# Optimization experiments

Measured on AMD Instinct MI355X. Metric: run time of the kernel, lower is better.

## Reference

```python
import jax, jax.numpy as jnp
import numpy as np

MARGIN = 0.2
EPS = 1e-6  # torch.pairwise_distance default eps added to (x1 - x2)


def setup_inputs() -> dict:
    key = jax.random.key(0)
    k1, k2 = jax.random.split(key)
    N, D = 8192, 128
    x = jax.random.normal(k1, (N, D), dtype=jnp.float32)
    target = jax.random.randint(k2, (N,), 0, 1000)
    return {"x": x, "target": target}


def _pairwise_dist(x):
    # torch.pairwise_distance(x.unsqueeze(0), x.unsqueeze(1)):
    #   diff[i, j] = x[j] - x[i] + EPS ; dist[i, j] = ||diff[i, j]||_2
    # Expanded quadratic form avoids the [N, N, D] diff tensor:
    #   ||a - b + e||^2 = ||a||^2 + ||b||^2 - 2 a.b + 2e*sum(a - b) + D*e^2
    sq = jnp.sum(x * x, axis=1)          # [N]
    s = jnp.sum(x, axis=1)               # [N]
    dot = x @ x.T                        # [N, N]
    D = x.shape[1]
    d2 = (sq[None, :] + sq[:, None] - 2.0 * dot
          + 2.0 * EPS * (s[None, :] - s[:, None]) + D * EPS * EPS)
    return jnp.sqrt(jnp.maximum(d2, 0.0))


def reference(x, target):
    N = x.shape[0]
    dist = _pairwise_dist(x)                                 # [N, N]
    same = target[None, :] == target[:, None]                # [N, N] bool
    pos_mask = (same & ~jnp.eye(N, dtype=bool)).astype(x.dtype)
    hardest_pos = jnp.max(pos_mask * dist, axis=1, keepdims=True)  # [N, 1]
    neg_mask = (~same).astype(x.dtype)
    max_neg = jnp.max(dist, axis=1, keepdims=True)           # [N, 1]
    anchor_neg = dist + max_neg * (1.0 - neg_mask)           # push positives up
    hardest_neg = jnp.min(anchor_neg, axis=1, keepdims=True) # [N, 1]
    loss = jax.nn.relu(hardest_pos - hardest_neg + MARGIN)
    return jnp.mean(loss)
```

## Files before the change

### kernel.cpp

```cpp
#include <hip/hip_runtime.h>

#define N 8192
#define Dk 128
#define EPSC 1e-6f
#define MARGIN 0.2f

typedef __attribute__((ext_vector_type(8))) short bf16x8;
typedef __attribute__((ext_vector_type(4))) float f32x4;

__device__ __forceinline__ unsigned short f2bf(float f) {
    unsigned u = __float_as_uint(f);
    u = (u + 0x7FFFu + ((u >> 16) & 1u)) >> 16;
    return (unsigned short)u;
}
__device__ __forceinline__ unsigned enc(float f) {
    unsigned u = __float_as_uint(f);
    return (u & 0x80000000u) ? ~u : (u | 0x80000000u);
}
__device__ __forceinline__ float dec(unsigned u) {
    return __uint_as_float((u & 0x80000000u) ? (u & 0x7FFFFFFFu) : ~u);
}

__device__ __forceinline__ void gl_lds16(const void* src, void* lds_dst) {
    __builtin_amdgcn_global_load_lds(
        (const __attribute__((address_space(1))) unsigned*)src,
        (__attribute__((address_space(3))) unsigned*)lds_dst, 16, 0, 0);
}

__global__ void prep_kernel(const float* __restrict__ x, const int* __restrict__ tgt,
                            unsigned short* __restrict__ Xb, uint2* __restrict__ QT,
                            float* __restrict__ P,
                            unsigned* __restrict__ wsHp, unsigned* __restrict__ wsMn) {
    int row = blockIdx.x * 4 + (threadIdx.x >> 6);
    int l = threadIdx.x & 63;
    const float2 v = *reinterpret_cast<const float2*>(&x[row * Dk + l * 2]);
    float sq = fmaf(v.x, v.x, v.y * v.y);
    float s = v.x + v.y;
    ushort2 a;
    a.x = f2bf(v.x);
    a.y = f2bf(v.y);
    int c_phys = (l >> 2) ^ (row & 7);
    *reinterpret_cast<ushort2*>(&Xb[row * Dk + c_phys * 8 + 2 * (l & 3)]) = a;
#pragma unroll
    for (int m = 32; m >= 1; m >>= 1) {
        sq += __shfl_xor(sq, m);
        s += __shfl_xor(s, m);
    }
    if (l == 0) {
        P[row] = sq - 2.0f * EPSC * s;
        float Qj = sq + 2.0f * EPSC * s + (float)Dk * EPSC * EPSC;
        uint2 qt;
        qt.x = __float_as_uint(-0.5f * Qj);
        qt.y = (unsigned)tgt[row];
        QT[row] = qt;
        wsHp[row] = 0xFF800000u;
        wsMn[row] = 0x007FFFFFu;
    }
}

__global__ __launch_bounds__(256, 4) void main_kernel(
        const unsigned short* __restrict__ Xb,
        const uint2* __restrict__ QT, const int* __restrict__ tgt,
        unsigned* __restrict__ wsHp, unsigned* __restrict__ wsMn) {
    __shared__ unsigned short Bs[2][64 * Dk];
    __shared__ uint2 QTs[2][128];

    const int tid = threadIdx.x;
    const int w = tid >> 6;
    const int lane = tid & 63;
    const int n = lane & 15;
    const int q = lane >> 4;
    const int sw = n & 7;

    const int ig = (int)blockIdx.x >> 4;
    const int js = (int)blockIdx.x & 15;
    const int rbase = ig * 128 + 32 * w;

    const bf16x8* Xv = reinterpret_cast<const bf16x8*>(Xb);

    bf16x8 Af[2][4];
#pragma unroll
    for (int ti = 0; ti < 2; ++ti)
#pragma unroll
        for (int kk = 0; kk < 4; ++kk)
            Af[ti][kk] = Xv[(rbase + 16 * ti + n) * 16 + ((q + 4 * kk) ^ sw)];

    int tsl[8];
#pragma unroll
    for (int ti = 0; ti < 2; ++ti) {
        int4 t4 = *reinterpret_cast<const int4*>(&tgt[rbase + 16 * ti + 4 * q]);
        tsl[4 * ti + 0] = t4.x;
        tsl[4 * ti + 1] = t4.y;
        tsl[4 * ti + 2] = t4.z;
        tsl[4 * ti + 3] = t4.w;
    }

    float hp[8], mn[8];
#pragma unroll
    for (int s = 0; s < 8; ++s) {
        hp[s] = INFINITY;
        mn[s] = -INFINITY;
    }

    auto stage = [&](int step) {
        const int jb = js * 512 + step * 64;
        const int buf = step & 1;
#pragma unroll
        for (int t = 0; t < 4; ++t)
            gl_lds16(&Xb[(jb + 16 * w + 4 * t) * Dk] + lane * 8,
                     &Bs[buf][(16 * w + 4 * t) * Dk]);
        if (w == 0)
            gl_lds16(reinterpret_cast<const unsigned short*>(&QT[jb]) + lane * 8,
                     &QTs[buf][0]);
    };

    stage(0);

    for (int step = 0; step < 8; ++step) {
        const int buf = step & 1;
        __syncthreads();
        if (step < 7) stage(step + 1);

        float Qv[4];
        int tv[4];
#pragma unroll
        for (int tj = 0; tj < 4; ++tj) {
            uint2 qt = QTs[buf][16 * tj + n];
            Qv[tj] = __uint_as_float(qt.x);
            tv[tj] = (int)qt.y;
        }

        f32x4 acc[2][4];
#pragma unroll
        for (int ti = 0; ti < 2; ++ti)
#pragma unroll
            for (int tj = 0; tj < 4; ++tj) acc[ti][tj] = Qv[tj];

#pragma unroll
        for (int kk = 0; kk < 4; ++kk) {
            bf16x8 Bf[4];
#pragma unroll
            for (int tj = 0; tj < 4; ++tj)
                Bf[tj] = *reinterpret_cast<const bf16x8*>(
                    &Bs[buf][(16 * tj + n) * Dk + (((q + 4 * kk) ^ sw) << 3)]);
#pragma unroll
            for (int ti = 0; ti < 2; ++ti)
#pragma unroll
                for (int tj = 0; tj < 4; ++tj)
                    acc[ti][tj] = __builtin_amdgcn_mfma_f32_16x16x32_bf16(Af[ti][kk], Bf[tj],
                                                                          acc[ti][tj], 0, 0, 0);
        }

#pragma unroll
        for (int tj = 0; tj < 4; ++tj) {
            int tvv = tv[tj];
#pragma unroll
            for (int ti = 0; ti < 2; ++ti) {
                f32x4 v = acc[ti][tj];
                int e0 = tvv == tsl[4 * ti + 0];
                int e1 = tvv == tsl[4 * ti + 1];
                int e2 = tvv == tsl[4 * ti + 2];
                int e3 = tvv == tsl[4 * ti + 3];
                if (__ballot(e0 | e1 | e2 | e3)) {
                    hp[4 * ti + 0] = fminf(hp[4 * ti + 0], e0 ? v[0] : INFINITY);
                    hp[4 * ti + 1] = fminf(hp[4 * ti + 1], e1 ? v[1] : INFINITY);
                    hp[4 * ti + 2] = fminf(hp[4 * ti + 2], e2 ? v[2] : INFINITY);
                    hp[4 * ti + 3] = fminf(hp[4 * ti + 3], e3 ? v[3] : INFINITY);
                    mn[4 * ti + 0] = fmaxf(mn[4 * ti + 0], e0 ? -INFINITY : v[0]);
                    mn[4 * ti + 1] = fmaxf(mn[4 * ti + 1], e1 ? -INFINITY : v[1]);
                    mn[4 * ti + 2] = fmaxf(mn[4 * ti + 2], e2 ? -INFINITY : v[2]);
                    mn[4 * ti + 3] = fmaxf(mn[4 * ti + 3], e3 ? -INFINITY : v[3]);
                } else {
                    mn[4 * ti + 0] = fmaxf(mn[4 * ti + 0], v[0]);
                    mn[4 * ti + 1] = fmaxf(mn[4 * ti + 1], v[1]);
                    mn[4 * ti + 2] = fmaxf(mn[4 * ti + 2], v[2]);
                    mn[4 * ti + 3] = fmaxf(mn[4 * ti + 3], v[3]);
                }
            }
        }
    }

#pragma unroll
    for (int m = 1; m <= 8; m <<= 1) {
#pragma unroll
        for (int s = 0; s < 8; ++s) {
            hp[s] = fminf(hp[s], __shfl_xor(hp[s], m));
            mn[s] = fmaxf(mn[s], __shfl_xor(mn[s], m));
        }
    }
    if (n == 0) {
#pragma unroll
        for (int ti = 0; ti < 2; ++ti) {
#pragma unroll
            for (int r = 0; r < 4; ++r) {
                int i = rbase + 16 * ti + 4 * q + r;
                atomicMin(&wsHp[i], enc(hp[4 * ti + r]));
                atomicMax(&wsMn[i], enc(mn[4 * ti + r]));
            }
        }
    }
}

__global__ void finish_kernel(const float* __restrict__ P,
                              const unsigned* __restrict__ wsHp,
                              const unsigned* __restrict__ wsMn,
                              float* __restrict__ out) {
    int t = threadIdx.x;
    float sum = 0.0f;
#pragma unroll
    for (int h = 0; h < 2; ++h) {
        int base = 8 * t + 4 * h;
        float4 Pv = *reinterpret_cast<const float4*>(&P[base]);
        uint4 Hv = *reinterpret_cast<const uint4*>(&wsHp[base]);
        uint4 Mv = *reinterpret_cast<const uint4*>(&wsMn[base]);
        const float* Pf = &Pv.x;
        const unsigned* Hu = &Hv.x;
        const unsigned* Mu = &Mv.x;
#pragma unroll
        for (int k = 0; k < 4; ++k) {
            float hp = sqrtf(fmaxf(fmaf(-2.0f, dec(Hu[k]), Pf[k]), 0.0f));
            float hn = sqrtf(fmaxf(fmaf(-2.0f, dec(Mu[k]), Pf[k]), 0.0f));
            sum += fmaxf(hp - hn + MARGIN, 0.0f);
        }
    }
#pragma unroll
    for (int m = 32; m >= 1; m >>= 1) sum += __shfl_xor(sum, m);
    __shared__ float ws[16];
    if ((t & 63) == 0) ws[t >> 6] = sum;
    __syncthreads();
    if (t == 0) {
        float tot = 0.0f;
#pragma unroll
        for (int i = 0; i < 16; ++i) tot += ws[i];
        out[0] = tot * (1.0f / (float)N);
    }
}

extern "C" void kernel_launch(void* const* d_in, const int* in_sizes, int n_in,
                              void* d_out, int out_size, void* d_ws, size_t ws_size,
                              hipStream_t stream) {
    const float* x = (const float*)d_in[0];
    const int* tgt = (const int*)d_in[1];
    float* out = (float*)d_out;

    char* ws = (char*)d_ws;
    const size_t xb = (size_t)N * Dk * 2;
    unsigned short* Xb = (unsigned short*)ws;
    uint2* QT = (uint2*)(ws + xb);
    float* P = (float*)(ws + xb + (size_t)N * 8);
    unsigned* wsHp = (unsigned*)(ws + xb + (size_t)N * 12);
    unsigned* wsMn = (unsigned*)(ws + xb + (size_t)N * 16);

    prep_kernel<<<N / 4, 256, 0, stream>>>(x, tgt, Xb, QT, P, wsHp, wsMn);
    main_kernel<<<1024, 256, 0, stream>>>(Xb, QT, tgt, wsHp, wsMn);
    finish_kernel<<<1, 1024, 0, stream>>>(P, wsHp, wsMn, out);
}
```

Baseline: 96.97 us.

## Replace LDS-staged B tiles with direct global register loads in single-wave blocks

Removes the shared-memory double buffer and __syncthreads, so each single-wave block loads B fragments straight from global (L2) memory into registers, with a two-deep register prefetch across k-steps. Each wave now covers 64 anchor rows instead of 32, which doubles A-fragment reuse per B load. The grid becomes 2048 blocks of 64 threads, and the XOR swizzle in the bf16 layout is dropped since LDS is no longer used. The aim is to cut LDS traffic and barrier overhead. In exchange, register pressure rises, global/L2 load traffic per MFMA is higher with no LDS sharing between waves, and occupancy may drop.

```diff
diff --git a/kernel.cpp b/kernel.cpp
--- a/kernel.cpp
+++ b/kernel.cpp
@@ -19,12 +19,6 @@
 }
 __device__ __forceinline__ float dec(unsigned u) {
     return __uint_as_float((u & 0x80000000u) ? (u & 0x7FFFFFFFu) : ~u);
-}
-
-__device__ __forceinline__ void gl_lds16(const void* src, void* lds_dst) {
-    __builtin_amdgcn_global_load_lds(
-        (const __attribute__((address_space(1))) unsigned*)src,
-        (__attribute__((address_space(3))) unsigned*)lds_dst, 16, 0, 0);
 }
 
 __global__ void prep_kernel(const float* __restrict__ x, const int* __restrict__ tgt,
@@ -39,8 +33,7 @@
     ushort2 a;
     a.x = f2bf(v.x);
     a.y = f2bf(v.y);
-    int c_phys = (l >> 2) ^ (row & 7);
-    *reinterpret_cast<ushort2*>(&Xb[row * Dk + c_phys * 8 + 2 * (l & 3)]) = a;
+    *reinterpret_cast<ushort2*>(&Xb[row * Dk + l * 2]) = a;
 #pragma unroll
     for (int m = 32; m >= 1; m >>= 1) {
         sq += __shfl_xor(sq, m);
@@ -58,36 +51,31 @@
     }
 }
 
-__global__ __launch_bounds__(256, 4) void main_kernel(
+__global__ __launch_bounds__(64, 2) void main_kernel(
         const unsigned short* __restrict__ Xb,
         const uint2* __restrict__ QT, const int* __restrict__ tgt,
         unsigned* __restrict__ wsHp, unsigned* __restrict__ wsMn) {
-    __shared__ unsigned short Bs[2][64 * Dk];
-    __shared__ uint2 QTs[2][128];
-
-    const int tid = threadIdx.x;
-    const int w = tid >> 6;
-    const int lane = tid & 63;
+    const int lane = threadIdx.x;
     const int n = lane & 15;
     const int q = lane >> 4;
-    const int sw = n & 7;
-
-    const int ig = (int)blockIdx.x >> 4;
+
+    const int rg = (int)blockIdx.x >> 4;
     const int js = (int)blockIdx.x & 15;
-    const int rbase = ig * 128 + 32 * w;
+    const int rbase = rg * 64;
+    const int jb0 = js * 512;
 
     const bf16x8* Xv = reinterpret_cast<const bf16x8*>(Xb);
 
-    bf16x8 Af[2][4];
-#pragma unroll
-    for (int ti = 0; ti < 2; ++ti)
+    bf16x8 Af[4][4];
+#pragma unroll
+    for (int ti = 0; ti < 4; ++ti)
 #pragma unroll
         for (int kk = 0; kk < 4; ++kk)
-            Af[ti][kk] = Xv[(rbase + 16 * ti + n) * 16 + ((q + 4 * kk) ^ sw)];
-
-    int tsl[8];
-#pragma unroll
-    for (int ti = 0; ti < 2; ++ti) {
+            Af[ti][kk] = Xv[(rbase + 16 * ti + n) * 16 + (q + 4 * kk)];
+
+    int tsl[16];
+#pragma unroll
+    for (int ti = 0; ti < 4; ++ti) {
         int4 t4 = *reinterpret_cast<const int4*>(&tgt[rbase + 16 * ti + 4 * q]);
         tsl[4 * ti + 0] = t4.x;
         tsl[4 * ti + 1] = t4.y;
@@ -95,67 +83,56 @@
         tsl[4 * ti + 3] = t4.w;
     }
 
-    float hp[8], mn[8];
-#pragma unroll
-    for (int s = 0; s < 8; ++s) {
+    float hp[16], mn[16];
+#pragma unroll
+    for (int s = 0; s < 16; ++s) {
         hp[s] = INFINITY;
         mn[s] = -INFINITY;
     }
 
-    auto stage = [&](int step) {
-        const int jb = js * 512 + step * 64;
-        const int buf = step & 1;
-#pragma unroll
-        for (int t = 0; t < 4; ++t)
-            gl_lds16(&Xb[(jb + 16 * w + 4 * t) * Dk] + lane * 8,
-                     &Bs[buf][(16 * w + 4 * t) * Dk]);
-        if (w == 0)
-            gl_lds16(reinterpret_cast<const unsigned short*>(&QT[jb]) + lane * 8,
-                     &QTs[buf][0]);
-    };
-
-    stage(0);
-
     for (int step = 0; step < 8; ++step) {
-        const int buf = step & 1;
-        __syncthreads();
-        if (step < 7) stage(step + 1);
+        const int jb = jb0 + step * 64;
 
         float Qv[4];
         int tv[4];
 #pragma unroll
         for (int tj = 0; tj < 4; ++tj) {
-            uint2 qt = QTs[buf][16 * tj + n];
+            uint2 qt = QT[jb + 16 * tj + n];
             Qv[tj] = __uint_as_float(qt.x);
             tv[tj] = (int)qt.y;
         }
 
-        f32x4 acc[2][4];
-#pragma unroll
-        for (int ti = 0; ti < 2; ++ti)
+        f32x4 acc[4][4];
+#pragma unroll
+        for (int ti = 0; ti < 4; ++ti)
 #pragma unroll
             for (int tj = 0; tj < 4; ++tj) acc[ti][tj] = Qv[tj];
 
+        bf16x8 Bf[2][4];
+#pragma unroll
+        for (int tj = 0; tj < 4; ++tj)
+            Bf[0][tj] = Xv[(jb + 16 * tj + n) * 16 + q];
 #pragma unroll
         for (int kk = 0; kk < 4; ++kk) {
-            bf16x8 Bf[4];
-#pragma unroll
-            for (int tj = 0; tj < 4; ++tj)
-                Bf[tj] = *reinterpret_cast<const bf16x8*>(
-                    &Bs[buf][(16 * tj + n) * Dk + (((q + 4 * kk) ^ sw) << 3)]);
-#pragma unroll
-            for (int ti = 0; ti < 2; ++ti)
+            const int cur = kk & 1;
+            if (kk < 3) {
 #pragma unroll
                 for (int tj = 0; tj < 4; ++tj)
-                    acc[ti][tj] = __builtin_amdgcn_mfma_f32_16x16x32_bf16(Af[ti][kk], Bf[tj],
-                                                                          acc[ti][tj], 0, 0, 0);
+                    Bf[cur ^ 1][tj] = Xv[(jb + 16 * tj + n) * 16 + (q + 4 * (kk + 1))];
+            }
+#pragma unroll
+            for (int ti = 0; ti < 4; ++ti)
+#pragma unroll
+                for (int tj = 0; tj < 4; ++tj)
+                    acc[ti][tj] = __builtin_amdgcn_mfma_f32_16x16x32_bf16(
+                        Af[ti][kk], Bf[cur][tj], acc[ti][tj], 0, 0, 0);
         }
 
 #pragma unroll
         for (int tj = 0; tj < 4; ++tj) {
             int tvv = tv[tj];
 #pragma unroll
-            for (int ti = 0; ti < 2; ++ti) {
+            for (int ti = 0; ti < 4; ++ti) {
                 f32x4 v = acc[ti][tj];
                 int e0 = tvv == tsl[4 * ti + 0];
                 int e1 = tvv == tsl[4 * ti + 1];
@@ -183,14 +160,14 @@
 #pragma unroll
     for (int m = 1; m <= 8; m <<= 1) {
 #pragma unroll
-        for (int s = 0; s < 8; ++s) {
+        for (int s = 0; s < 16; ++s) {
             hp[s] = fminf(hp[s], __shfl_xor(hp[s], m));
             mn[s] = fmaxf(mn[s], __shfl_xor(mn[s], m));
         }
     }
     if (n == 0) {
 #pragma unroll
-        for (int ti = 0; ti < 2; ++ti) {
+        for (int ti = 0; ti < 4; ++ti) {
 #pragma unroll
             for (int r = 0; r < 4; ++r) {
                 int i = rbase + 16 * ti + 4 * q + r;
@@ -252,6 +229,6 @@
     unsigned* wsMn = (unsigned*)(ws + xb + (size_t)N * 16);
 
     prep_kernel<<<N / 4, 256, 0, stream>>>(x, tgt, Xb, QT, P, wsHp, wsMn);
-    main_kernel<<<1024, 256, 0, stream>>>(Xb, QT, tgt, wsHp, wsMn);
+    main_kernel<<<2048, 64, 0, stream>>>(Xb, QT, tgt, wsHp, wsMn);
     finish_kernel<<<1, 1024, 0, stream>>>(P, wsHp, wsMn, out);
 }
```

After: 111.2 us. 14.6% more time.

## Exploit distance symmetry with triangular 128x128 tile grid and column-side reductions

Applied to the files above, without the earlier changes.

Switches from a full 64x512 block tiling over the N×N distance matrix to a triangular grid of 128x128 tiles (2080 blocks), computing each off-diagonal tile once and reducing it both row-wise and column-wise, so the matrix multiply work is roughly halved. The column reductions are adjusted by each row's Q term and pushed to the global hardest-positive and hardest-negative arrays with extra atomics. The whole B tile is now loaded once instead of double-buffered. MFMA sections are wrapped in setprio, and occupancy drops to 3 blocks per CU. The trade-off is more epilogue ALU work, more shuffles and atomics, and a larger LDS footprint per block.

```diff
diff --git a/kernel.cpp b/kernel.cpp
--- a/kernel.cpp
+++ b/kernel.cpp
@@ -58,12 +58,11 @@
     }
 }
 
-__global__ __launch_bounds__(256, 4) void main_kernel(
-        const unsigned short* __restrict__ Xb,
-        const uint2* __restrict__ QT, const int* __restrict__ tgt,
+__global__ __launch_bounds__(256, 3) void main_kernel(
+        const unsigned short* __restrict__ Xb, const uint2* __restrict__ QT,
         unsigned* __restrict__ wsHp, unsigned* __restrict__ wsMn) {
-    __shared__ unsigned short Bs[2][64 * Dk];
-    __shared__ uint2 QTs[2][128];
+    __shared__ unsigned short Bs[128 * Dk];
+    __shared__ uint2 QTs[128];
 
     const int tid = threadIdx.x;
     const int w = tid >> 6;
@@ -72,11 +71,25 @@
     const int q = lane >> 4;
     const int sw = n & 7;
 
-    const int ig = (int)blockIdx.x >> 4;
-    const int js = (int)blockIdx.x & 15;
+    int t = (int)blockIdx.x;
+    int jg = (int)((sqrtf(8.0f * (float)t + 1.0f) - 1.0f) * 0.5f);
+    while ((jg + 1) * (jg + 2) / 2 <= t) ++jg;
+    while (jg * (jg + 1) / 2 > t) --jg;
+    const int ig = t - jg * (jg + 1) / 2;
+    const bool diag = (ig == jg);
+
     const int rbase = ig * 128 + 32 * w;
+    const int jbase = jg * 128;
 
     const bf16x8* Xv = reinterpret_cast<const bf16x8*>(Xb);
+
+#pragma unroll
+    for (int tt = 0; tt < 8; ++tt)
+        gl_lds16(&Xb[(jbase + 32 * w + 4 * tt) * Dk] + lane * 8,
+                 &Bs[(32 * w + 4 * tt) * Dk]);
+    if (w == 0)
+        gl_lds16(reinterpret_cast<const unsigned short*>(&QT[jbase]) + lane * 8,
+                 &QTs[0]);
 
     bf16x8 Af[2][4];
 #pragma unroll
@@ -85,14 +98,20 @@
         for (int kk = 0; kk < 4; ++kk)
             Af[ti][kk] = Xv[(rbase + 16 * ti + n) * 16 + ((q + 4 * kk) ^ sw)];
 
+    float qi[8];
     int tsl[8];
 #pragma unroll
     for (int ti = 0; ti < 2; ++ti) {
-        int4 t4 = *reinterpret_cast<const int4*>(&tgt[rbase + 16 * ti + 4 * q]);
-        tsl[4 * ti + 0] = t4.x;
-        tsl[4 * ti + 1] = t4.y;
-        tsl[4 * ti + 2] = t4.z;
-        tsl[4 * ti + 3] = t4.w;
+        uint4 a = *reinterpret_cast<const uint4*>(&QT[rbase + 16 * ti + 4 * q]);
+        uint4 b = *reinterpret_cast<const uint4*>(&QT[rbase + 16 * ti + 4 * q + 2]);
+        qi[4 * ti + 0] = __uint_as_float(a.x);
+        tsl[4 * ti + 0] = (int)a.y;
+        qi[4 * ti + 1] = __uint_as_float(a.z);
+        tsl[4 * ti + 1] = (int)a.w;
+        qi[4 * ti + 2] = __uint_as_float(b.x);
+        tsl[4 * ti + 2] = (int)b.y;
+        qi[4 * ti + 3] = __uint_as_float(b.z);
+        tsl[4 * ti + 3] = (int)b.w;
     }
 
     float hp[8], mn[8];
@@ -101,31 +120,29 @@
         hp[s] = INFINITY;
         mn[s] = -INFINITY;
     }
-
-    auto stage = [&](int step) {
-        const int jb = js * 512 + step * 64;
-        const int buf = step & 1;
-#pragma unroll
-        for (int t = 0; t < 4; ++t)
-            gl_lds16(&Xb[(jb + 16 * w + 4 * t) * Dk] + lane * 8,
-                     &Bs[buf][(16 * w + 4 * t) * Dk]);
-        if (w == 0)
-            gl_lds16(reinterpret_cast<const unsigned short*>(&QT[jb]) + lane * 8,
-                     &QTs[buf][0]);
-    };
-
-    stage(0);
-
-    for (int step = 0; step < 8; ++step) {
-        const int buf = step & 1;
-        __syncthreads();
-        if (step < 7) stage(step + 1);
-
+    float cmx[2][4], chp[2][4];
+#pragma unroll
+    for (int h = 0; h < 2; ++h)
+#pragma unroll
+        for (int tj = 0; tj < 4; ++tj) {
+            cmx[h][tj] = -INFINITY;
+            chp[h][tj] = INFINITY;
+        }
+
+    const char* LdsBase = reinterpret_cast<const char*>(&Bs[0]);
+    unsigned lb[4];
+#pragma unroll
+    for (int kk = 0; kk < 4; ++kk) lb[kk] = n * 256 + (((q + 4 * kk) ^ sw) << 4);
+
+    __syncthreads();
+
+#pragma unroll
+    for (int h = 0; h < 2; ++h) {
         float Qv[4];
         int tv[4];
 #pragma unroll
         for (int tj = 0; tj < 4; ++tj) {
-            uint2 qt = QTs[buf][16 * tj + n];
+            uint2 qt = QTs[h * 64 + 16 * tj + n];
             Qv[tj] = __uint_as_float(qt.x);
             tv[tj] = (int)qt.y;
         }
@@ -142,13 +159,15 @@
 #pragma unroll
             for (int tj = 0; tj < 4; ++tj)
                 Bf[tj] = *reinterpret_cast<const bf16x8*>(
-                    &Bs[buf][(16 * tj + n) * Dk + (((q + 4 * kk) ^ sw) << 3)]);
+                    LdsBase + lb[kk] + h * 16384 + tj * 4096);
+            __builtin_amdgcn_s_setprio(1);
 #pragma unroll
             for (int ti = 0; ti < 2; ++ti)
 #pragma unroll
                 for (int tj = 0; tj < 4; ++tj)
-                    acc[ti][tj] = __builtin_amdgcn_mfma_f32_16x16x32_bf16(Af[ti][kk], Bf[tj],
-                                                                          acc[ti][tj], 0, 0, 0);
+                    acc[ti][tj] = __builtin_amdgcn_mfma_f32_16x16x32_bf16(
+                        Af[ti][kk], Bf[tj], acc[ti][tj], 0, 0, 0);
+            __builtin_amdgcn_s_setprio(0);
         }
 
 #pragma unroll
@@ -170,11 +189,32 @@
                     mn[4 * ti + 1] = fmaxf(mn[4 * ti + 1], e1 ? -INFINITY : v[1]);
                     mn[4 * ti + 2] = fmaxf(mn[4 * ti + 2], e2 ? -INFINITY : v[2]);
                     mn[4 * ti + 3] = fmaxf(mn[4 * ti + 3], e3 ? -INFINITY : v[3]);
+                    if (!diag) {
+                        float t0 = v[0] + qi[4 * ti + 0];
+                        float t1 = v[1] + qi[4 * ti + 1];
+                        float t2 = v[2] + qi[4 * ti + 2];
+                        float t3 = v[3] + qi[4 * ti + 3];
+                        cmx[h][tj] = fmaxf(cmx[h][tj], e0 ? -INFINITY : t0);
+                        cmx[h][tj] = fmaxf(cmx[h][tj], e1 ? -INFINITY : t1);
+                        cmx[h][tj] = fmaxf(cmx[h][tj], e2 ? -INFINITY : t2);
+                        cmx[h][tj] = fmaxf(cmx[h][tj], e3 ? -INFINITY : t3);
+                        chp[h][tj] = fminf(chp[h][tj], e0 ? t0 : INFINITY);
+                        chp[h][tj] = fminf(chp[h][tj], e1 ? t1 : INFINITY);
+                        chp[h][tj] = fminf(chp[h][tj], e2 ? t2 : INFINITY);
+                        chp[h][tj] = fminf(chp[h][tj], e3 ? t3 : INFINITY);
+                    }
                 } else {
                     mn[4 * ti + 0] = fmaxf(mn[4 * ti + 0], v[0]);
                     mn[4 * ti + 1] = fmaxf(mn[4 * ti + 1], v[1]);
                     mn[4 * ti + 2] = fmaxf(mn[4 * ti + 2], v[2]);
                     mn[4 * ti + 3] = fmaxf(mn[4 * ti + 3], v[3]);
+                    if (!diag) {
+                        float t0 = v[0] + qi[4 * ti + 0];
+                        float t1 = v[1] + qi[4 * ti + 1];
+                        float t2 = v[2] + qi[4 * ti + 2];
+                        float t3 = v[3] + qi[4 * ti + 3];
+                        cmx[h][tj] = fmaxf(cmx[h][tj], fmaxf(fmaxf(t0, t1), fmaxf(t2, t3)));
+                    }
                 }
             }
         }
@@ -190,13 +230,36 @@
     }
     if (n == 0) {
 #pragma unroll
-        for (int ti = 0; ti < 2; ++ti) {
+        for (int ti = 0; ti < 2; ++ti)
 #pragma unroll
             for (int r = 0; r < 4; ++r) {
                 int i = rbase + 16 * ti + 4 * q + r;
-                atomicMin(&wsHp[i], enc(hp[4 * ti + r]));
+                if (hp[4 * ti + r] < 3.0e38f) atomicMin(&wsHp[i], enc(hp[4 * ti + r]));
                 atomicMax(&wsMn[i], enc(mn[4 * ti + r]));
             }
+    }
+
+    if (!diag) {
+#pragma unroll
+        for (int h = 0; h < 2; ++h)
+#pragma unroll
+            for (int tj = 0; tj < 4; ++tj) {
+                cmx[h][tj] = fmaxf(cmx[h][tj], __shfl_xor(cmx[h][tj], 16));
+                cmx[h][tj] = fmaxf(cmx[h][tj], __shfl_xor(cmx[h][tj], 32));
+                chp[h][tj] = fminf(chp[h][tj], __shfl_xor(chp[h][tj], 16));
+                chp[h][tj] = fminf(chp[h][tj], __shfl_xor(chp[h][tj], 32));
+            }
+        if (q == 0) {
+#pragma unroll
+            for (int h = 0; h < 2; ++h)
+#pragma unroll
+                for (int tj = 0; tj < 4; ++tj) {
+                    int j = jbase + h * 64 + 16 * tj + n;
+                    float Qvh = __uint_as_float(QTs[h * 64 + 16 * tj + n].x);
+                    atomicMax(&wsMn[j], enc(cmx[h][tj] - Qvh));
+                    if (chp[h][tj] < 3.0e38f)
+                        atomicMin(&wsHp[j], enc(chp[h][tj] - Qvh));
+                }
         }
     }
 }
@@ -252,6 +315,6 @@
     unsigned* wsMn = (unsigned*)(ws + xb + (size_t)N * 16);
 
     prep_kernel<<<N / 4, 256, 0, stream>>>(x, tgt, Xb, QT, P, wsHp, wsMn);
-    main_kernel<<<1024, 256, 0, stream>>>(Xb, QT, tgt, wsHp, wsMn);
+    main_kernel<<<2080, 256, 0, stream>>>(Xb, QT, wsHp, wsMn);
     finish_kernel<<<1, 1024, 0, stream>>>(P, wsHp, wsMn, out);
 }
```

Result: slower. 99.01 us (+2.1%).

## Replace LDS-staged B tiles with per-wave register double-buffered global loads

Applied to the files above, without the earlier changes.

The main kernel now runs one wave per block (4096 blocks of 64 threads) and loads B tiles straight from global memory into registers, alternating between two buffers, instead of staging them through shared memory with async global-to-LDS copies and block barriers. Each step covers 32 columns, so there are 16 steps per wave. The MFMA section is wrapped in s_setprio to favour the matrix work. This removes the __syncthreads and LDS traffic, but B data is no longer shared across the 4 waves of a block, so global/L2 reads of B go up about fourfold and register pressure rises.

```diff
diff --git a/kernel.cpp b/kernel.cpp
--- a/kernel.cpp
+++ b/kernel.cpp
@@ -19,12 +19,6 @@
 }
 __device__ __forceinline__ float dec(unsigned u) {
     return __uint_as_float((u & 0x80000000u) ? (u & 0x7FFFFFFFu) : ~u);
-}
-
-__device__ __forceinline__ void gl_lds16(const void* src, void* lds_dst) {
-    __builtin_amdgcn_global_load_lds(
-        (const __attribute__((address_space(1))) unsigned*)src,
-        (__attribute__((address_space(3))) unsigned*)lds_dst, 16, 0, 0);
 }
 
 __global__ void prep_kernel(const float* __restrict__ x, const int* __restrict__ tgt,
@@ -58,23 +52,20 @@
     }
 }
 
-__global__ __launch_bounds__(256, 4) void main_kernel(
+__global__ __launch_bounds__(64, 3) void main_kernel(
         const unsigned short* __restrict__ Xb,
         const uint2* __restrict__ QT, const int* __restrict__ tgt,
         unsigned* __restrict__ wsHp, unsigned* __restrict__ wsMn) {
-    __shared__ unsigned short Bs[2][64 * Dk];
-    __shared__ uint2 QTs[2][128];
-
-    const int tid = threadIdx.x;
-    const int w = tid >> 6;
-    const int lane = tid & 63;
+    const int lane = threadIdx.x;
     const int n = lane & 15;
     const int q = lane >> 4;
     const int sw = n & 7;
 
-    const int ig = (int)blockIdx.x >> 4;
-    const int js = (int)blockIdx.x & 15;
-    const int rbase = ig * 128 + 32 * w;
+    const int wid = (int)blockIdx.x;
+    const int rg = wid >> 4;
+    const int cs = wid & 15;
+    const int rbase = rg * 32;
+    const int jb0 = cs * 512;
 
     const bf16x8* Xv = reinterpret_cast<const bf16x8*>(Xb);
 
@@ -102,57 +93,52 @@
         mn[s] = -INFINITY;
     }
 
-    auto stage = [&](int step) {
-        const int jb = js * 512 + step * 64;
-        const int buf = step & 1;
-#pragma unroll
-        for (int t = 0; t < 4; ++t)
-            gl_lds16(&Xb[(jb + 16 * w + 4 * t) * Dk] + lane * 8,
-                     &Bs[buf][(16 * w + 4 * t) * Dk]);
-        if (w == 0)
-            gl_lds16(reinterpret_cast<const unsigned short*>(&QT[jb]) + lane * 8,
-                     &QTs[buf][0]);
+    bf16x8 BpA[4][2], BpB[4][2];
+    uint2 qtA[2], qtB[2];
+
+    auto loadB = [&](int s, bf16x8(&Bp)[4][2], uint2(&qt)[2]) {
+        const int jb = jb0 + s * 32;
+#pragma unroll
+        for (int kk = 0; kk < 4; ++kk)
+#pragma unroll
+            for (int tj = 0; tj < 2; ++tj)
+                Bp[kk][tj] = Xv[(jb + 16 * tj + n) * 16 + ((q + 4 * kk) ^ sw)];
+#pragma unroll
+        for (int tj = 0; tj < 2; ++tj) qt[tj] = QT[jb + 16 * tj + n];
     };
 
-    stage(0);
-
-    for (int step = 0; step < 8; ++step) {
-        const int buf = step & 1;
-        __syncthreads();
-        if (step < 7) stage(step + 1);
-
-        float Qv[4];
-        int tv[4];
-#pragma unroll
-        for (int tj = 0; tj < 4; ++tj) {
-            uint2 qt = QTs[buf][16 * tj + n];
-            Qv[tj] = __uint_as_float(qt.x);
-            tv[tj] = (int)qt.y;
-        }
-
-        f32x4 acc[2][4];
+    auto STEP = [&](int s, bf16x8(&Bp)[4][2], uint2(&qt)[2]) {
+        float Qv[2];
+        int tv[2];
+#pragma unroll
+        for (int tj = 0; tj < 2; ++tj) {
+            Qv[tj] = __uint_as_float(qt[tj].x);
+            tv[tj] = (int)qt[tj].y;
+        }
+
+        f32x4 acc[2][2];
 #pragma unroll
         for (int ti = 0; ti < 2; ++ti)
 #pragma unroll
-            for (int tj = 0; tj < 4; ++tj) acc[ti][tj] = Qv[tj];
-
-#pragma unroll
-        for (int kk = 0; kk < 4; ++kk) {
-            bf16x8 Bf[4];
-#pragma unroll
-            for (int tj = 0; tj < 4; ++tj)
-                Bf[tj] = *reinterpret_cast<const bf16x8*>(
-                    &Bs[buf][(16 * tj + n) * Dk + (((q + 4 * kk) ^ sw) << 3)]);
+            for (int tj = 0; tj < 2; ++tj) acc[ti][tj] = Qv[tj];
+
+        __builtin_amdgcn_s_setprio(1);
+#pragma unroll
+        for (int kk = 0; kk < 4; ++kk)
 #pragma unroll
             for (int ti = 0; ti < 2; ++ti)
 #pragma unroll
-                for (int tj = 0; tj < 4; ++tj)
-                    acc[ti][tj] = __builtin_amdgcn_mfma_f32_16x16x32_bf16(Af[ti][kk], Bf[tj],
-                                                                          acc[ti][tj], 0, 0, 0);
-        }
-
-#pragma unroll
-        for (int tj = 0; tj < 4; ++tj) {
+                for (int tj = 0; tj < 2; ++tj)
+                    acc[ti][tj] = __builtin_amdgcn_mfma_f32_16x16x32_bf16(
+                        Af[ti][kk], Bp[kk][tj], acc[ti][tj], 0, 0, 0);
+        __builtin_amdgcn_s_setprio(0);
+
+        if (s + 2 < 16) loadB(s + 2, Bp, qt);
+
+        const int jb = jb0 + s * 32;
+        (void)jb;
+#pragma unroll
+        for (int tj = 0; tj < 2; ++tj) {
             int tvv = tv[tj];
 #pragma unroll
             for (int ti = 0; ti < 2; ++ti) {
@@ -178,6 +164,14 @@
                 }
             }
         }
+    };
+
+    loadB(0, BpA, qtA);
+    loadB(1, BpB, qtB);
+
+    for (int s = 0; s < 16; s += 2) {
+        STEP(s, BpA, qtA);
+        STEP(s + 1, BpB, qtB);
     }
 
 #pragma unroll
@@ -252,6 +246,6 @@
     unsigned* wsMn = (unsigned*)(ws + xb + (size_t)N * 16);
 
     prep_kernel<<<N / 4, 256, 0, stream>>>(x, tgt, Xb, QT, P, wsHp, wsMn);
-    main_kernel<<<1024, 256, 0, stream>>>(Xb, QT, tgt, wsHp, wsMn);
+    main_kernel<<<4096, 64, 0, stream>>>(Xb, QT, tgt, wsHp, wsMn);
     finish_kernel<<<1, 1024, 0, stream>>>(P, wsHp, wsMn, out);
 }
```

After: 126.4 us. 1.3x slower.
